# Kernel optimization log

Measured on AMD Instinct MI355X. Metric: run time of the kernel, lower is better.

## Reference

```python
import jax, jax.numpy as jnp
import numpy as np

N_HEAD = 16  # matches init_kwargs n_head


def setup_inputs() -> dict:
    key = jax.random.key(0)
    ks = jax.random.split(key, 8)
    B, T, D = 8, 1024, 1024
    x = jax.random.normal(ks[0], (B, T, D), dtype=jnp.float32)
    # causal additive mask, as built by Whisper: upper-triangular -inf
    mask = jnp.triu(jnp.full((T, T), -jnp.inf, dtype=jnp.float32), k=1)
    s = 0.02
    Wq = jax.random.normal(ks[1], (D, D), dtype=jnp.float32) * s
    bq = jax.random.normal(ks[2], (D,), dtype=jnp.float32) * s
    Wk = jax.random.normal(ks[3], (D, D), dtype=jnp.float32) * s
    Wv = jax.random.normal(ks[4], (D, D), dtype=jnp.float32) * s
    bv = jax.random.normal(ks[5], (D,), dtype=jnp.float32) * s
    Wo = jax.random.normal(ks[6], (D, D), dtype=jnp.float32) * s
    bo = jax.random.normal(ks[7], (D,), dtype=jnp.float32) * s
    return {"x": x, "mask": mask, "Wq": Wq, "bq": bq, "Wk": Wk,
            "Wv": Wv, "bv": bv, "Wo": Wo, "bo": bo}


def reference(x, mask, Wq, bq, Wk, Wv, bv, Wo, bo):
    B, T, D = x.shape
    H = N_HEAD
    hd = D // H
    scale = hd ** -0.25  # applied to both q and k, as in the torch code
    q = (x @ Wq.T + bq).reshape(B, T, H, hd).transpose(0, 2, 1, 3) * scale
    k = (x @ Wk.T).reshape(B, T, H, hd).transpose(0, 2, 1, 3) * scale
    v = (x @ Wv.T + bv).reshape(B, T, H, hd).transpose(0, 2, 1, 3)
    # [B,H,T,T] scores + causal additive mask (self-attn, non-cross branch)
    qk = jnp.einsum('bhqd,bhkd->bhqk', q, k) + mask[:T, :T]
    qk = qk.astype(jnp.float32)  # fp32 softmax as in original
    w = jax.nn.softmax(qk, axis=-1).astype(x.dtype)
    wv = jnp.einsum('bhqk,bhkd->bhqd', w, v).transpose(0, 2, 1, 3).reshape(B, T, D)
    out = wv @ Wo.T + bo
    return out, qk
```

## Files before the change

### kernel.cpp

```cpp
#include <hip/hip_runtime.h>
#include <stdint.h>

typedef __attribute__((ext_vector_type(8))) short bf16x8;
typedef __attribute__((ext_vector_type(4))) float f32x4;

typedef __attribute__((address_space(1))) const void* gvp;
typedef __attribute__((address_space(3))) void* lvp;
#define GLOAD16(g, l) __builtin_amdgcn_global_load_lds((gvp)(g), (lvp)(l), 16, 0, 0)

#define MASKV (-3.0e38f)

__device__ __forceinline__ ushort f2bf(float f) {
  uint32_t u = __float_as_uint(f);
  u += 0x7fff + ((u >> 16) & 1);
  return (ushort)(u >> 16);
}

__global__ __launch_bounds__(256) void cvt_kernel(const float* __restrict__ src,
                                                  ushort* __restrict__ dst, int n4) {
  int i = blockIdx.x * 256 + threadIdx.x;
  if (i >= n4) return;
  float4 v = reinterpret_cast<const float4*>(src)[i];
  ushort4 o;
  o.x = f2bf(v.x); o.y = f2bf(v.y); o.z = f2bf(v.z); o.w = f2bf(v.w);
  reinterpret_cast<ushort4*>(dst)[i] = o;
}

__global__ __launch_bounds__(256) void cvt_weights(
    const float* __restrict__ Wq, const float* __restrict__ Wk,
    const float* __restrict__ Wv, const float* __restrict__ Wo,
    ushort* __restrict__ wqkv, ushort* __restrict__ wob) {
  int wsel = blockIdx.x >> 10;
  int i = (blockIdx.x & 1023) * 256 + threadIdx.x;
  const float* src = wsel == 0 ? Wq : wsel == 1 ? Wk : wsel == 2 ? Wv : Wo;
  ushort* dst = wsel == 0 ? wqkv : wsel == 1 ? (wqkv + 1048576)
              : wsel == 2 ? (wqkv + 2097152) : wob;
  float4 v = reinterpret_cast<const float4*>(src)[i];
  ushort4 o;
  o.x = f2bf(v.x); o.y = f2bf(v.y); o.z = f2bf(v.z); o.w = f2bf(v.w);
  reinterpret_cast<ushort4*>(dst)[i] = o;
}

__global__ __launch_bounds__(256) void gemm_bt(
    const ushort* __restrict__ A, const ushort* __restrict__ B,
    int K, int ldc, int mode,
    const float* __restrict__ biasA, const float* __restrict__ biasB,
    float scale, ushort* __restrict__ outb, float* __restrict__ outf) {
  __shared__ ushort As[128 * 32];
  __shared__ ushort Bs[128 * 32];
  const int tid = threadIdx.x;
  const int lane = tid & 63, wid = tid >> 6;
  const int lr = lane & 15, lg = lane >> 4;
  const int wr = wid >> 1, wc = wid & 1;
  const ushort* Ab = A + (size_t)blockIdx.x * 128 * K;
  const ushort* Bb = B + (size_t)blockIdx.y * 128 * K;
  f32x4 acc[4][4];
#pragma unroll
  for (int i = 0; i < 4; ++i)
#pragma unroll
    for (int j = 0; j < 4; ++j) acc[i][j] = (f32x4){0.f, 0.f, 0.f, 0.f};

  for (int k0 = 0; k0 < K; k0 += 32) {
#pragma unroll
    for (int t = 0; t < 2; ++t) {
      int c = tid + t * 256;
      int row = c >> 2, cc = c & 3;
      GLOAD16(Ab + (size_t)row * K + k0 + cc * 8, &As[c * 8]);
      GLOAD16(Bb + (size_t)row * K + k0 + cc * 8, &Bs[c * 8]);
    }
    __syncthreads();
    bf16x8 af[4], bfr[4];
#pragma unroll
    for (int i = 0; i < 4; ++i) {
      af[i]  = *(const bf16x8*)&As[(wr * 64 + i * 16 + lr) * 32 + lg * 8];
      bfr[i] = *(const bf16x8*)&Bs[(wc * 64 + i * 16 + lr) * 32 + lg * 8];
    }
#pragma unroll
    for (int mi = 0; mi < 4; ++mi)
#pragma unroll
      for (int ni = 0; ni < 4; ++ni)
        acc[mi][ni] = __builtin_amdgcn_mfma_f32_16x16x32_bf16(bfr[ni], af[mi], acc[mi][ni], 0, 0, 0);
    __syncthreads();
  }

  const int m0 = blockIdx.x * 128 + wr * 64;
  const int n0 = blockIdx.y * 128 + wc * 64;
#pragma unroll
  for (int mi = 0; mi < 4; ++mi) {
    int m = m0 + mi * 16 + lr;
#pragma unroll
    for (int ni = 0; ni < 4; ++ni) {
      int nbase = n0 + ni * 16 + lg * 4;
      if (mode == 0) {
        int which = nbase >> 10, nn = nbase & 1023;
        float4 ba;
        ushort4 o;
        if (which == 0) {
          ba = *reinterpret_cast<const float4*>(&biasA[nn]);
          o.x = f2bf((acc[mi][ni][0] + ba.x) * scale);
          o.y = f2bf((acc[mi][ni][1] + ba.y) * scale);
          o.z = f2bf((acc[mi][ni][2] + ba.z) * scale);
          o.w = f2bf((acc[mi][ni][3] + ba.w) * scale);
        } else if (which == 1) {
          o.x = f2bf(acc[mi][ni][0] * scale);
          o.y = f2bf(acc[mi][ni][1] * scale);
          o.z = f2bf(acc[mi][ni][2] * scale);
          o.w = f2bf(acc[mi][ni][3] * scale);
        } else {
          ba = *reinterpret_cast<const float4*>(&biasB[nn]);
          o.x = f2bf(acc[mi][ni][0] + ba.x);
          o.y = f2bf(acc[mi][ni][1] + ba.y);
          o.z = f2bf(acc[mi][ni][2] + ba.z);
          o.w = f2bf(acc[mi][ni][3] + ba.w);
        }
        *reinterpret_cast<ushort4*>(&outb[(size_t)m * ldc + nbase]) = o;
      } else {
        float4 ba = *reinterpret_cast<const float4*>(&biasA[nbase]);
        f32x4 o;
        o[0] = acc[mi][ni][0] + ba.x;
        o[1] = acc[mi][ni][1] + ba.y;
        o[2] = acc[mi][ni][2] + ba.z;
        o[3] = acc[mi][ni][3] + ba.w;
        *reinterpret_cast<f32x4*>(&outf[(size_t)m * ldc + nbase]) = o;
      }
    }
  }
}

__global__ __launch_bounds__(256) void vtrans_kernel(const ushort* __restrict__ qkvb,
                                                     ushort* __restrict__ vt) {
  const int tt = blockIdx.x;
  const int bh = blockIdx.y;
  const int b = bh >> 4, h = bh & 15;
  __shared__ ushort Ts[64 * 64];
  const int tid = threadIdx.x;
  const ushort* src = qkvb + (size_t)(b * 1024 + tt * 64) * 3072 + 2048 + h * 64;
#pragma unroll
  for (int p = 0; p < 2; ++p) {
    int idx = tid + p * 256;
    int tr = idx >> 3, cc = idx & 7;
    bf16x8 vv = *(const bf16x8*)(src + (size_t)tr * 3072 + cc * 8);
#pragma unroll
    for (int j = 0; j < 8; ++j) {
      int d = cc * 8 + j;
      Ts[d * 64 + (((tr >> 3) ^ (d & 7)) << 3) + (tr & 7)] = (ushort)vv[j];
    }
  }
  __syncthreads();
  ushort* dst = vt + (size_t)bh * 64 * 1024 + tt * 64;
#pragma unroll
  for (int p = 0; p < 2; ++p) {
    int idx = tid + p * 256;
    int dr = idx >> 3, tc = idx & 7;
    bf16x8 row = *(const bf16x8*)&Ts[dr * 64 + ((tc ^ (dr & 7)) << 3)];
    *(bf16x8*)(dst + (size_t)dr * 1024 + tc * 8) = row;
  }
}

__global__ __launch_bounds__(256) void attn_kernel(
    const ushort* __restrict__ qkv, const ushort* __restrict__ vt,
    float* __restrict__ qk_out, ushort* __restrict__ wv) {
  const int bh = blockIdx.x;
  const int qt = 15 - blockIdx.y;
  const int b = bh >> 4, h = bh & 15;
  const int tid = threadIdx.x;
  const int lane = tid & 63, w = tid >> 6;
  const int lr = lane & 15, lg = lane >> 4;

  __shared__ ushort Ks[2][64 * 64];
  __shared__ ushort Vs[2][64 * 64];
  __shared__ ushort Ps[64 * 64];

  const ushort* Qb = qkv + (size_t)(b * 1024 + qt * 64) * 3072 + h * 64;
  bf16x8 qf[2];
#pragma unroll
  for (int ks = 0; ks < 2; ++ks)
    qf[ks] = *(const bf16x8*)(Qb + (size_t)(w * 16 + lr) * 3072 + lg * 8 + ks * 32);

  const ushort* Kb  = qkv + (size_t)b * 1024 * 3072 + 1024 + h * 64;
  const ushort* Vtb = vt + (size_t)bh * 64 * 1024;

  float m_run = -INFINITY, l_run = 0.f;
  f32x4 oacc[4];
#pragma unroll
  for (int i = 0; i < 4; ++i) oacc[i] = (f32x4){0.f, 0.f, 0.f, 0.f};

  float* qkb = qk_out + ((size_t)bh << 20) + (size_t)qt * 64 * 1024;
  const int qglob = qt * 64 + w * 16 + lr;

  auto stage = [&](int kt, int bi) {
#pragma unroll
    for (int t = 0; t < 2; ++t) {
      int c = tid + t * 256;
      int row = c >> 3, pos = c & 7;
      int g = pos ^ (row & 7);
      GLOAD16(Kb + (size_t)(kt * 64 + row) * 3072 + g * 8, &Ks[bi][c * 8]);
      GLOAD16(Vtb + (size_t)row * 1024 + kt * 64 + g * 8, &Vs[bi][c * 8]);
    }
  };

  stage(0, 0);
  for (int kt = 0; kt <= qt; ++kt) {
    const int cur = kt & 1;
    __syncthreads();
    if (kt < qt) stage(kt + 1, cur ^ 1);

    f32x4 sacc[4];
#pragma unroll
    for (int i = 0; i < 4; ++i) sacc[i] = (f32x4){0.f, 0.f, 0.f, 0.f};
#pragma unroll
    for (int ks = 0; ks < 2; ++ks)
#pragma unroll
      for (int ni = 0; ni < 4; ++ni) {
        int row = ni * 16 + lr;
        int cch = (lg + ks * 4) ^ (row & 7);
        bf16x8 kf = *(const bf16x8*)&Ks[cur][row * 64 + cch * 8];
        sacc[ni] = __builtin_amdgcn_mfma_f32_16x16x32_bf16(kf, qf[ks], sacc[ni], 0, 0, 0);
      }

    float mx = -INFINITY;
    if (kt == qt) {
#pragma unroll
      for (int ni = 0; ni < 4; ++ni)
#pragma unroll
        for (int r = 0; r < 4; ++r) {
          int kglob = kt * 64 + ni * 16 + lg * 4 + r;
          float s2 = sacc[ni][r];
          if (kglob > qglob) { s2 = MASKV; sacc[ni][r] = s2; }
          mx = fmaxf(mx, s2);
        }
    } else {
#pragma unroll
      for (int ni = 0; ni < 4; ++ni)
#pragma unroll
        for (int r = 0; r < 4; ++r) mx = fmaxf(mx, sacc[ni][r]);
    }

#pragma unroll
    for (int ni = 0; ni < 4; ++ni)
      *reinterpret_cast<f32x4*>(&qkb[(size_t)(w * 16 + lr) * 1024 + kt * 64 + ni * 16 + lg * 4]) = sacc[ni];

    mx = fmaxf(mx, __shfl_xor(mx, 16));
    mx = fmaxf(mx, __shfl_xor(mx, 32));

    float mn = fmaxf(m_run, mx);
    float alpha = __expf(m_run - mn);
    m_run = mn;

    float psum = 0.f;
    const int prow = w * 16 + lr;
#pragma unroll
    for (int ni = 0; ni < 4; ++ni) {
      float p0 = __expf(sacc[ni][0] - m_run);
      float p1 = __expf(sacc[ni][1] - m_run);
      float p2 = __expf(sacc[ni][2] - m_run);
      float p3 = __expf(sacc[ni][3] - m_run);
      psum += (p0 + p1) + (p2 + p3);
      ushort4 pk;
      pk.x = f2bf(p0); pk.y = f2bf(p1); pk.z = f2bf(p2); pk.w = f2bf(p3);
      int colc = ((ni * 2 + (lg >> 1)) ^ (prow & 7));
      *reinterpret_cast<ushort4*>(&Ps[prow * 64 + colc * 8 + (lg & 1) * 4]) = pk;
    }
    psum += __shfl_xor(psum, 16);
    psum += __shfl_xor(psum, 32);
    l_run = l_run * alpha + psum;
#pragma unroll
    for (int ni = 0; ni < 4; ++ni)
#pragma unroll
      for (int r = 0; r < 4; ++r) oacc[ni][r] *= alpha;

#pragma unroll
    for (int ks = 0; ks < 2; ++ks) {
      int pch = (lg + ks * 4) ^ (lr & 7);
      bf16x8 pa = *(const bf16x8*)&Ps[(w * 16 + lr) * 64 + pch * 8];
#pragma unroll
      for (int ni = 0; ni < 4; ++ni) {
        int vrow = ni * 16 + lr;
        int vch = (lg + ks * 4) ^ (vrow & 7);
        bf16x8 vb = *(const bf16x8*)&Vs[cur][vrow * 64 + vch * 8];
        oacc[ni] = __builtin_amdgcn_mfma_f32_16x16x32_bf16(vb, pa, oacc[ni], 0, 0, 0);
      }
    }
  }

  if (qt < 15) {
    int c0 = (qt + 1) * 16;
    int nc = 256 - c0;
    int total = 64 * nc;
    f32x4 mv = (f32x4){MASKV, MASKV, MASKV, MASKV};
    for (int i = tid; i < total; i += 256) {
      int r = i / nc, c = i % nc;
      __builtin_nontemporal_store(mv,
          reinterpret_cast<f32x4*>(qkb + (size_t)r * 1024) + c0 + c);
    }
  }

  {
    float inv = 1.f / l_run;
    ushort* wvp = wv + (size_t)(b * 1024 + qt * 64 + w * 16 + lr) * 1024 + h * 64;
#pragma unroll
    for (int ni = 0; ni < 4; ++ni) {
      ushort4 ov;
      ov.x = f2bf(oacc[ni][0] * inv);
      ov.y = f2bf(oacc[ni][1] * inv);
      ov.z = f2bf(oacc[ni][2] * inv);
      ov.w = f2bf(oacc[ni][3] * inv);
      *reinterpret_cast<ushort4*>(&wvp[ni * 16 + lg * 4]) = ov;
    }
  }
}

extern "C" void kernel_launch(void* const* d_in, const int* in_sizes, int n_in,
                              void* d_out, int out_size, void* d_ws, size_t ws_size,
                              hipStream_t stream) {
  const float* x  = (const float*)d_in[0];
  const float* Wq = (const float*)d_in[2];
  const float* bq = (const float*)d_in[3];
  const float* Wk = (const float*)d_in[4];
  const float* Wv = (const float*)d_in[5];
  const float* bv = (const float*)d_in[6];
  const float* Wo = (const float*)d_in[7];
  const float* bo = (const float*)d_in[8];

  float* out = (float*)d_out;
  float* qk  = out + (size_t)8 * 1024 * 1024;

  ushort* xb   = (ushort*)d_ws;
  ushort* wqkv = xb + 8388608;
  ushort* wob  = wqkv + 3145728;
  ushort* qkvb = wob + 1048576;
  ushort* wvb  = qkvb + 25165824;
  ushort* vtb  = xb;

  cvt_kernel<<<8192, 256, 0, stream>>>(x, xb, 2097152);
  cvt_weights<<<4096, 256, 0, stream>>>(Wq, Wk, Wv, Wo, wqkv, wob);

  const float scale = 0.35355339059327373f;
  gemm_bt<<<dim3(64, 24), 256, 0, stream>>>(xb, wqkv, 1024, 3072, 0, bq, bv, scale, qkvb, nullptr);
  vtrans_kernel<<<dim3(16, 128), 256, 0, stream>>>(qkvb, vtb);
  attn_kernel<<<dim3(128, 16), 256, 0, stream>>>(qkvb, vtb, qk, wvb);
  gemm_bt<<<dim3(64, 8), 256, 0, stream>>>(wvb, wob, 1024, 1024, 1, bo, nullptr, 1.0f, nullptr, out);
}
```

Measured before the change: 274.1 us.

## Fuse V transpose into QKV GEMM epilogue and merge conversion kernels

```diff
diff --git a/kernel.cpp b/kernel.cpp
--- a/kernel.cpp
+++ b/kernel.cpp
@@ -16,36 +16,37 @@
   return (ushort)(u >> 16);
 }
 
-__global__ __launch_bounds__(256) void cvt_kernel(const float* __restrict__ src,
-                                                  ushort* __restrict__ dst, int n4) {
+__global__ __launch_bounds__(256) void cvt_all(
+    const float* __restrict__ x,
+    const float* __restrict__ Wq, const float* __restrict__ Wk,
+    const float* __restrict__ Wv, const float* __restrict__ Wo,
+    ushort* __restrict__ xb, ushort* __restrict__ wqkv,
+    ushort* __restrict__ wob) {
   int i = blockIdx.x * 256 + threadIdx.x;
-  if (i >= n4) return;
-  float4 v = reinterpret_cast<const float4*>(src)[i];
+  const float* src;
+  ushort* dst;
+  int off;
+  if (i < 2097152) { src = x; dst = xb; off = i; }
+  else {
+    int j = i - 2097152;
+    int wsel = j >> 18, idx = j & 262143;
+    src = wsel == 0 ? Wq : wsel == 1 ? Wk : wsel == 2 ? Wv : Wo;
+    dst = wsel == 0 ? wqkv : wsel == 1 ? (wqkv + 1048576)
+        : wsel == 2 ? (wqkv + 2097152) : wob;
+    off = idx;
+  }
+  float4 v = reinterpret_cast<const float4*>(src)[off];
   ushort4 o;
   o.x = f2bf(v.x); o.y = f2bf(v.y); o.z = f2bf(v.z); o.w = f2bf(v.w);
-  reinterpret_cast<ushort4*>(dst)[i] = o;
-}
-
-__global__ __launch_bounds__(256) void cvt_weights(
-    const float* __restrict__ Wq, const float* __restrict__ Wk,
-    const float* __restrict__ Wv, const float* __restrict__ Wo,
-    ushort* __restrict__ wqkv, ushort* __restrict__ wob) {
-  int wsel = blockIdx.x >> 10;
-  int i = (blockIdx.x & 1023) * 256 + threadIdx.x;
-  const float* src = wsel == 0 ? Wq : wsel == 1 ? Wk : wsel == 2 ? Wv : Wo;
-  ushort* dst = wsel == 0 ? wqkv : wsel == 1 ? (wqkv + 1048576)
-              : wsel == 2 ? (wqkv + 2097152) : wob;
-  float4 v = reinterpret_cast<const float4*>(src)[i];
-  ushort4 o;
-  o.x = f2bf(v.x); o.y = f2bf(v.y); o.z = f2bf(v.z); o.w = f2bf(v.w);
-  reinterpret_cast<ushort4*>(dst)[i] = o;
+  reinterpret_cast<ushort4*>(dst)[off] = o;
 }
 
 __global__ __launch_bounds__(256) void gemm_bt(
     const ushort* __restrict__ A, const ushort* __restrict__ B,
     int K, int ldc, int mode,
     const float* __restrict__ biasA, const float* __restrict__ biasB,
-    float scale, ushort* __restrict__ outb, float* __restrict__ outf) {
+    float scale, ushort* __restrict__ outb, ushort* __restrict__ vt,
+    float* __restrict__ outf) {
   __shared__ ushort As[128 * 32];
   __shared__ ushort Bs[128 * 32];
   const int tid = threadIdx.x;
@@ -93,27 +94,31 @@
       int nbase = n0 + ni * 16 + lg * 4;
       if (mode == 0) {
         int which = nbase >> 10, nn = nbase & 1023;
-        float4 ba;
-        ushort4 o;
         if (which == 0) {
-          ba = *reinterpret_cast<const float4*>(&biasA[nn]);
+          float4 ba = *reinterpret_cast<const float4*>(&biasA[nn]);
+          ushort4 o;
           o.x = f2bf((acc[mi][ni][0] + ba.x) * scale);
           o.y = f2bf((acc[mi][ni][1] + ba.y) * scale);
           o.z = f2bf((acc[mi][ni][2] + ba.z) * scale);
           o.w = f2bf((acc[mi][ni][3] + ba.w) * scale);
+          *reinterpret_cast<ushort4*>(&outb[(size_t)m * ldc + nn]) = o;
         } else if (which == 1) {
+          ushort4 o;
           o.x = f2bf(acc[mi][ni][0] * scale);
           o.y = f2bf(acc[mi][ni][1] * scale);
           o.z = f2bf(acc[mi][ni][2] * scale);
           o.w = f2bf(acc[mi][ni][3] * scale);
+          *reinterpret_cast<ushort4*>(&outb[(size_t)m * ldc + 1024 + nn]) = o;
         } else {
-          ba = *reinterpret_cast<const float4*>(&biasB[nn]);
-          o.x = f2bf(acc[mi][ni][0] + ba.x);
-          o.y = f2bf(acc[mi][ni][1] + ba.y);
-          o.z = f2bf(acc[mi][ni][2] + ba.z);
-          o.w = f2bf(acc[mi][ni][3] + ba.w);
+          float4 ba = *reinterpret_cast<const float4*>(&biasB[nn]);
+          int h2 = nn >> 6, d2 = nn & 63;
+          int b2 = m >> 10, t2 = m & 1023;
+          size_t vbase = ((size_t)((b2 * 16 + h2) * 64 + d2)) * 1024 + t2;
+          vt[vbase]        = f2bf(acc[mi][ni][0] + ba.x);
+          vt[vbase + 1024] = f2bf(acc[mi][ni][1] + ba.y);
+          vt[vbase + 2048] = f2bf(acc[mi][ni][2] + ba.z);
+          vt[vbase + 3072] = f2bf(acc[mi][ni][3] + ba.w);
         }
-        *reinterpret_cast<ushort4*>(&outb[(size_t)m * ldc + nbase]) = o;
       } else {
         float4 ba = *reinterpret_cast<const float4*>(&biasA[nbase]);
         f32x4 o;
@@ -127,36 +132,6 @@
   }
 }
 
-__global__ __launch_bounds__(256) void vtrans_kernel(const ushort* __restrict__ qkvb,
-                                                     ushort* __restrict__ vt) {
-  const int tt = blockIdx.x;
-  const int bh = blockIdx.y;
-  const int b = bh >> 4, h = bh & 15;
-  __shared__ ushort Ts[64 * 64];
-  const int tid = threadIdx.x;
-  const ushort* src = qkvb + (size_t)(b * 1024 + tt * 64) * 3072 + 2048 + h * 64;
-#pragma unroll
-  for (int p = 0; p < 2; ++p) {
-    int idx = tid + p * 256;
-    int tr = idx >> 3, cc = idx & 7;
-    bf16x8 vv = *(const bf16x8*)(src + (size_t)tr * 3072 + cc * 8);
-#pragma unroll
-    for (int j = 0; j < 8; ++j) {
-      int d = cc * 8 + j;
-      Ts[d * 64 + (((tr >> 3) ^ (d & 7)) << 3) + (tr & 7)] = (ushort)vv[j];
-    }
-  }
-  __syncthreads();
-  ushort* dst = vt + (size_t)bh * 64 * 1024 + tt * 64;
-#pragma unroll
-  for (int p = 0; p < 2; ++p) {
-    int idx = tid + p * 256;
-    int dr = idx >> 3, tc = idx & 7;
-    bf16x8 row = *(const bf16x8*)&Ts[dr * 64 + ((tc ^ (dr & 7)) << 3)];
-    *(bf16x8*)(dst + (size_t)dr * 1024 + tc * 8) = row;
-  }
-}
-
 __global__ __launch_bounds__(256) void attn_kernel(
     const ushort* __restrict__ qkv, const ushort* __restrict__ vt,
     float* __restrict__ qk_out, ushort* __restrict__ wv) {
@@ -171,13 +146,13 @@
   __shared__ ushort Vs[2][64 * 64];
   __shared__ ushort Ps[64 * 64];
 
-  const ushort* Qb = qkv + (size_t)(b * 1024 + qt * 64) * 3072 + h * 64;
+  const ushort* Qb = qkv + (size_t)(b * 1024 + qt * 64) * 2048 + h * 64;
   bf16x8 qf[2];
 #pragma unroll
   for (int ks = 0; ks < 2; ++ks)
-    qf[ks] = *(const bf16x8*)(Qb + (size_t)(w * 16 + lr) * 3072 + lg * 8 + ks * 32);
-
-  const ushort* Kb  = qkv + (size_t)b * 1024 * 3072 + 1024 + h * 64;
+    qf[ks] = *(const bf16x8*)(Qb + (size_t)(w * 16 + lr) * 2048 + lg * 8 + ks * 32);
+
+  const ushort* Kb  = qkv + (size_t)b * 1024 * 2048 + 1024 + h * 64;
   const ushort* Vtb = vt + (size_t)bh * 64 * 1024;
 
   float m_run = -INFINITY, l_run = 0.f;
@@ -194,7 +169,7 @@
       int c = tid + t * 256;
       int row = c >> 3, pos = c & 7;
       int g = pos ^ (row & 7);
-      GLOAD16(Kb + (size_t)(kt * 64 + row) * 3072 + g * 8, &Ks[bi][c * 8]);
+      GLOAD16(Kb + (size_t)(kt * 64 + row) * 2048 + g * 8, &Ks[bi][c * 8]);
       GLOAD16(Vtb + (size_t)row * 1024 + kt * 64 + g * 8, &Vs[bi][c * 8]);
     }
   };
@@ -329,15 +304,13 @@
   ushort* wqkv = xb + 8388608;
   ushort* wob  = wqkv + 3145728;
   ushort* qkvb = wob + 1048576;
-  ushort* wvb  = qkvb + 25165824;
-  ushort* vtb  = xb;
-
-  cvt_kernel<<<8192, 256, 0, stream>>>(x, xb, 2097152);
-  cvt_weights<<<4096, 256, 0, stream>>>(Wq, Wk, Wv, Wo, wqkv, wob);
+  ushort* vtb  = qkvb + 16777216;
+  ushort* wvb  = vtb + 8388608;
+
+  cvt_all<<<12288, 256, 0, stream>>>(x, Wq, Wk, Wv, Wo, xb, wqkv, wob);
 
   const float scale = 0.35355339059327373f;
-  gemm_bt<<<dim3(64, 24), 256, 0, stream>>>(xb, wqkv, 1024, 3072, 0, bq, bv, scale, qkvb, nullptr);
-  vtrans_kernel<<<dim3(16, 128), 256, 0, stream>>>(qkvb, vtb);
+  gemm_bt<<<dim3(64, 24), 256, 0, stream>>>(xb, wqkv, 1024, 2048, 0, bq, bv, scale, qkvb, vtb, nullptr);
   attn_kernel<<<dim3(128, 16), 256, 0, stream>>>(qkvb, vtb, qk, wvb);
-  gemm_bt<<<dim3(64, 8), 256, 0, stream>>>(wvb, wob, 1024, 1024, 1, bo, nullptr, 1.0f, nullptr, out);
-}
+  gemm_bt<<<dim3(64, 8), 256, 0, stream>>>(wvb, wob, 1024, 1024, 1, bo, nullptr, 1.0f, nullptr, nullptr, out);
+}
```

Result: faster. 260.6 us (-4.9%).
